# Kernel tuning notes

Hardware: AMD Instinct MI355X
Metric: run time of the kernel (lower is better)

Reference implementation:

```python
import jax, jax.numpy as jnp
import numpy as np
from jax import lax

TOP_K = 8
EPS = 1e-12


def l2_normalize(x, axis):
    sq = jnp.sum(x * x, axis=axis, keepdims=True)
    return x * lax.rsqrt(jnp.maximum(sq, EPS))


def setup_inputs() -> dict:
    key = jax.random.key(0)
    k1, k2, k3, k4 = jax.random.split(key, 4)
    B, N, C = 256, 197, 768
    POOL, LEN = 1024, 8
    x_embed = jax.random.normal(k1, (B, N, C), dtype=jnp.float32)
    prompt = jax.random.uniform(k2, (POOL, LEN, C), dtype=jnp.float32, minval=-1.0, maxval=1.0)
    prompt_key = jax.random.uniform(k3, (POOL, C), dtype=jnp.float32, minval=-1.0, maxval=1.0)
    # kaiming_normal fan_out: std = sqrt(2 / fan_out)
    proj_w = jax.random.normal(k4, (C, C), dtype=jnp.float32) * np.sqrt(2.0 / C).astype(np.float32)
    proj_b = jnp.zeros((C,), dtype=jnp.float32)
    return {"x_embed": x_embed, "prompt": prompt, "prompt_key": prompt_key,
            "proj_w": proj_w, "proj_b": proj_b}


def reference(x_embed, prompt, prompt_key, proj_w, proj_b):
    B = x_embed.shape[0]
    # embedding_key == 'mean'
    x_mean = jnp.mean(x_embed, axis=1)                     # [B, C]
    prompt_norm = l2_normalize(prompt_key, axis=1)         # [P, C]
    x_norm = l2_normalize(x_mean, axis=1)                  # [B, C]
    similarity = x_norm @ prompt_norm.T                    # [B, P]
    _, idx = lax.top_k(similarity, TOP_K)                  # [B, K]
    # gather prompts: [B, K, L, C] -> [B, K*L, C]
    bp = prompt[idx]
    Bk, K, L, C = bp.shape
    batched_prompt = bp.reshape(Bk, K * L, C)
    # projection + residual (dropout in eval mode = identity)
    batched_prompt = batched_prompt @ proj_w.T + proj_b + batched_prompt
    # key loss term
    batched_key_norm = prompt_norm[idx]                    # [B, K, C]
    reduce_sim = jnp.sum(batched_key_norm * x_norm[:, None, :]) / B
    prompted = jnp.concatenate([x_embed[:, :1, :], batched_prompt, x_embed[:, 1:, :]], axis=1)
    return prompted, reduce_sim
```

## Files before the change

kernel.cpp:

```cpp
#include <hip/hip_runtime.h>
#include <float.h>
#include <math.h>

#define B_    256
#define N_    197
#define C_    768
#define POOL_ 1024
#define LEN_  8
#define TOPK_ 8
#define PROWS (POOL_*LEN_)
#define OUTROWS 261

typedef __attribute__((ext_vector_type(8))) short short8_t;
typedef __attribute__((ext_vector_type(4))) float f32x4;

static const size_t OFF_XMEAN = 0;
static const size_t OFF_XNORM = 786432;
static const size_t OFF_PNORM = 1572864;
static const size_t OFF_SIM   = 4718592;
static const size_t OFF_IDX   = 5767168;
static const size_t OFF_ACC   = 5775360;
static const size_t OFF_ABF   = 5775616;
static const size_t OFF_WBF   = 18358528;
static const size_t OFF_PROJ  = 19538176;

__global__ __launch_bounds__(256) void k1_mean_copy(const float* __restrict__ x,
                                                    float* __restrict__ out,
                                                    float* __restrict__ xmean) {
    int b   = blockIdx.x / 3;
    int seg = blockIdx.x % 3;
    int t = threadIdx.x;
    int r = t >> 6;
    int c = t & 63;
    int c4 = seg * 64 + c;
    const float4* xin  = (const float4*)x   + (size_t)b * (N_ * 192) + c4;
    float4*       outb = (float4*)out       + (size_t)b * (OUTROWS * 192) + c4;

    float sx = 0.f, sy = 0.f, sz = 0.f, sw = 0.f;
    #pragma unroll 7
    for (int n = r; n < 196; n += 4) {
        float4 v = xin[(size_t)n * 192];
        sx += v.x; sy += v.y; sz += v.z; sw += v.w;
        int orow = (n == 0) ? 0 : (64 + n);
        outb[(size_t)orow * 192] = v;
    }
    if (r == 0) {
        float4 v = xin[(size_t)196 * 192];
        sx += v.x; sy += v.y; sz += v.z; sw += v.w;
        outb[(size_t)260 * 192] = v;
    }
    __shared__ float4 red[4][64];
    float4 s; s.x = sx; s.y = sy; s.z = sz; s.w = sw;
    red[r][c] = s;
    __syncthreads();
    if (r == 0) {
        float4 a = red[0][c], b2 = red[1][c], c2 = red[2][c], d = red[3][c];
        const float inv = 1.0f / (float)N_;
        float4 m;
        m.x = (a.x + b2.x + c2.x + d.x) * inv;
        m.y = (a.y + b2.y + c2.y + d.y) * inv;
        m.z = (a.z + b2.z + c2.z + d.z) * inv;
        m.w = (a.w + b2.w + c2.w + d.w) * inv;
        ((float4*)xmean)[b * 192 + c4] = m;
    }
}

__global__ __launch_bounds__(256) void k2_normalize(const float* __restrict__ xmean,
                                                    const float* __restrict__ pkey,
                                                    float* __restrict__ xnorm,
                                                    float* __restrict__ pnorm,
                                                    float* __restrict__ sim_accum) {
    __shared__ float red[256];
    int r = blockIdx.x;
    const float* src; float* dst;
    if (r < B_) { src = xmean + (size_t)r * C_; dst = xnorm + (size_t)r * C_; }
    else        { src = pkey  + (size_t)(r - B_) * C_; dst = pnorm + (size_t)(r - B_) * C_; }
    int t = threadIdx.x;
    float v0 = src[t], v1 = src[t + 256], v2 = src[t + 512];
    red[t] = v0*v0 + v1*v1 + v2*v2;
    __syncthreads();
    for (int off = 128; off > 0; off >>= 1) {
        if (t < off) red[t] += red[t + off];
        __syncthreads();
    }
    float inv = 1.0f / sqrtf(fmaxf(red[0], 1e-12f));
    dst[t] = v0 * inv; dst[t + 256] = v1 * inv; dst[t + 512] = v2 * inv;
    if (r == 0 && t == 0) sim_accum[0] = 0.0f;
}

__device__ __forceinline__ unsigned short f2bf(float f) {
    unsigned int u = __float_as_uint(f);
    u += 0x7fffu + ((u >> 16) & 1u);
    return (unsigned short)(u >> 16);
}
__global__ __launch_bounds__(256) void k2b_convert(const float* __restrict__ prompt,
                                                   const float* __restrict__ projw,
                                                   unsigned short* __restrict__ Abf,
                                                   unsigned short* __restrict__ Wbf) {
    int i4 = blockIdx.x * 256 + threadIdx.x;
    float4 v; unsigned short* d;
    if (i4 < (PROWS * C_ / 4)) {
        v = ((const float4*)prompt)[i4];
        d = Abf + (size_t)i4 * 4;
    } else {
        int j4 = i4 - PROWS * C_ / 4;
        v = ((const float4*)projw)[j4];
        d = Wbf + (size_t)j4 * 4;
    }
    ushort4 o; o.x = f2bf(v.x); o.y = f2bf(v.y); o.z = f2bf(v.z); o.w = f2bf(v.w);
    *(ushort4*)d = o;
}

__global__ __launch_bounds__(256) void k3_sim(const float* __restrict__ xnorm,
                                              const float* __restrict__ pnorm,
                                              float* __restrict__ sim) {
    __shared__ float As[32][33];
    __shared__ float Bs[32][33];
    int t = threadIdx.x;
    int m0 = blockIdx.y * 32, n0 = blockIdx.x * 32;
    int lrow = t >> 3, lc = (t & 7) * 4;
    int ty = t >> 4, tx = t & 15;
    float a00 = 0.f, a01 = 0.f, a10 = 0.f, a11 = 0.f;
    for (int k0 = 0; k0 < C_; k0 += 32) {
        float4 va = *(const float4*)&xnorm[(size_t)(m0 + lrow) * C_ + k0 + lc];
        float4 vb = *(const float4*)&pnorm[(size_t)(n0 + lrow) * C_ + k0 + lc];
        __syncthreads();
        As[lrow][lc] = va.x; As[lrow][lc+1] = va.y; As[lrow][lc+2] = va.z; As[lrow][lc+3] = va.w;
        Bs[lrow][lc] = vb.x; Bs[lrow][lc+1] = vb.y; Bs[lrow][lc+2] = vb.z; Bs[lrow][lc+3] = vb.w;
        __syncthreads();
        #pragma unroll
        for (int kk = 0; kk < 32; ++kk) {
            float a0 = As[ty*2][kk],   a1 = As[ty*2+1][kk];
            float b0 = Bs[tx*2][kk],   b1 = Bs[tx*2+1][kk];
            a00 += a0*b0; a01 += a0*b1; a10 += a1*b0; a11 += a1*b1;
        }
    }
    sim[(size_t)(m0 + ty*2    ) * POOL_ + n0 + tx*2    ] = a00;
    sim[(size_t)(m0 + ty*2    ) * POOL_ + n0 + tx*2 + 1] = a01;
    sim[(size_t)(m0 + ty*2 + 1) * POOL_ + n0 + tx*2    ] = a10;
    sim[(size_t)(m0 + ty*2 + 1) * POOL_ + n0 + tx*2 + 1] = a11;
}

__global__ __launch_bounds__(256) void k4_topk(const float* __restrict__ sim,
                                               int* __restrict__ idx,
                                               float* __restrict__ sim_accum) {
    __shared__ float vals[POOL_];
    __shared__ float wv[4];
    __shared__ int   wi[4];
    int b = blockIdx.x, t = threadIdx.x;
    int wave = t >> 6;
    #pragma unroll
    for (int i = 0; i < 4; ++i) vals[t + 256*i] = sim[(size_t)b * POOL_ + t + 256*i];
    __syncthreads();
    float sumv = 0.0f;
    for (int k = 0; k < TOPK_; ++k) {
        float bv = -FLT_MAX; int bi = POOL_;
        #pragma unroll
        for (int i = 0; i < 4; ++i) {
            int n = t + 256*i;
            float v = vals[n];
            if (v > bv) { bv = v; bi = n; }
        }
        #pragma unroll
        for (int off = 32; off > 0; off >>= 1) {
            float v2 = __shfl_down(bv, off);
            int   i2 = __shfl_down(bi, off);
            if (v2 > bv || (v2 == bv && i2 < bi)) { bv = v2; bi = i2; }
        }
        if ((t & 63) == 0) { wv[wave] = bv; wi[wave] = bi; }
        __syncthreads();
        if (t == 0) {
            float fv = wv[0]; int fi = wi[0];
            #pragma unroll
            for (int w = 1; w < 4; ++w) {
                float v2 = wv[w]; int i2 = wi[w];
                if (v2 > fv || (v2 == fv && i2 < fi)) { fv = v2; fi = i2; }
            }
            idx[b*TOPK_ + k] = fi;
            sumv += fv;
            vals[fi] = -FLT_MAX;
        }
        __syncthreads();
    }
    if (t == 0) atomicAdd(sim_accum, sumv);
}

__global__ __launch_bounds__(256) void k5_gemm(const unsigned short* __restrict__ A,
                                               const unsigned short* __restrict__ W,
                                               const float* __restrict__ bias,
                                               const float* __restrict__ resid,
                                               float* __restrict__ out) {
    __shared__ short As[64*32];
    __shared__ short Bs[128*32];
    const int tid = threadIdx.x;
    const int m0 = blockIdx.y * 64, n0 = blockIdx.x * 128;
    const int wave = tid >> 6, lane = tid & 63;
    const int quad = lane >> 4, lr = lane & 15;
    const int srow = tid >> 2;
    const int scol = (tid & 3) * 8;

    f32x4 acc[4][2] = {};

    for (int kt = 0; kt < 24; ++kt) {
        const int k0 = kt * 32;
        __syncthreads();
        __builtin_amdgcn_global_load_lds(
            (const __attribute__((address_space(1))) void*)&A[(size_t)(m0 + srow) * C_ + k0 + scol],
            (__attribute__((address_space(3))) void*)&As[srow*32 + scol], 16, 0, 0);
        __builtin_amdgcn_global_load_lds(
            (const __attribute__((address_space(1))) void*)&W[(size_t)(n0 + srow) * C_ + k0 + scol],
            (__attribute__((address_space(3))) void*)&Bs[srow*32 + scol], 16, 0, 0);
        __builtin_amdgcn_global_load_lds(
            (const __attribute__((address_space(1))) void*)&W[(size_t)(n0 + 64 + srow) * C_ + k0 + scol],
            (__attribute__((address_space(3))) void*)&Bs[(64 + srow)*32 + scol], 16, 0, 0);
        __syncthreads();

        short8_t af[4], bf[2];
        #pragma unroll
        for (int i = 0; i < 4; ++i)
            af[i] = *(const short8_t*)&As[(i*16 + lr)*32 + quad*8];
        #pragma unroll
        for (int j = 0; j < 2; ++j)
            bf[j] = *(const short8_t*)&Bs[(wave*32 + j*16 + lr)*32 + quad*8];
        #pragma unroll
        for (int i = 0; i < 4; ++i)
            #pragma unroll
            for (int j = 0; j < 2; ++j)
                acc[i][j] = __builtin_amdgcn_mfma_f32_16x16x32_bf16(af[i], bf[j], acc[i][j], 0, 0, 0);
    }

    #pragma unroll
    for (int j = 0; j < 2; ++j) {
        const int n = n0 + wave*32 + j*16 + lr;
        const float bn = bias[n];
        #pragma unroll
        for (int i = 0; i < 4; ++i) {
            const int mbase = m0 + i*16 + quad*4;
            #pragma unroll
            for (int r = 0; r < 4; ++r) {
                const int m = mbase + r;
                out[(size_t)m * C_ + n] = acc[i][j][r] + bn + resid[(size_t)m * C_ + n];
            }
        }
    }
}

__global__ __launch_bounds__(64) void k6_gather(const float* __restrict__ projall,
                                                const int* __restrict__ idx,
                                                const float* __restrict__ sim_accum,
                                                float* __restrict__ out) {
    int row = blockIdx.x;
    int b = row >> 6, j = row & 63;
    int k = j >> 3, l = j & 7;
    int p = idx[b * TOPK_ + k];
    const float4* src = (const float4*)projall + (size_t)(p * LEN_ + l) * 192;
    float4* dst = (float4*)out + (size_t)(b * OUTROWS + 1 + j) * 192;
    int t = threadIdx.x;
    dst[t]       = src[t];
    dst[t + 64]  = src[t + 64];
    dst[t + 128] = src[t + 128];
    if (row == 0 && t == 0)
        out[(size_t)B_ * OUTROWS * C_] = sim_accum[0] * (1.0f / (float)B_);
}

extern "C" void kernel_launch(void* const* d_in, const int* in_sizes, int n_in,
                              void* d_out, int out_size, void* d_ws, size_t ws_size,
                              hipStream_t stream) {
    const float* x_embed = (const float*)d_in[0];
    const float* prompt  = (const float*)d_in[1];
    const float* pkey    = (const float*)d_in[2];
    const float* projw   = (const float*)d_in[3];
    const float* projb   = (const float*)d_in[4];
    float* out = (float*)d_out;
    char* ws = (char*)d_ws;

    float*          xmean   = (float*)(ws + OFF_XMEAN);
    float*          xnorm   = (float*)(ws + OFF_XNORM);
    float*          pnorm   = (float*)(ws + OFF_PNORM);
    float*          sim     = (float*)(ws + OFF_SIM);
    int*            idxp    = (int*)(ws + OFF_IDX);
    float*          acc     = (float*)(ws + OFF_ACC);
    unsigned short* Abf     = (unsigned short*)(ws + OFF_ABF);
    unsigned short* Wbf     = (unsigned short*)(ws + OFF_WBF);
    float*          projall = (float*)(ws + OFF_PROJ);

    k1_mean_copy<<<B_ * 3, 256, 0, stream>>>(x_embed, out, xmean);
    k2_normalize<<<B_ + POOL_, 256, 0, stream>>>(xmean, pkey, xnorm, pnorm, acc);
    k2b_convert<<<(PROWS * C_ / 4 + 768 * 768 / 4) / 256, 256, 0, stream>>>(prompt, projw, Abf, Wbf);
    k3_sim<<<dim3(POOL_ / 32, B_ / 32), 256, 0, stream>>>(xnorm, pnorm, sim);
    k4_topk<<<B_, 256, 0, stream>>>(sim, idxp, acc);
    k5_gemm<<<dim3(C_ / 128, PROWS / 64), 256, 0, stream>>>(Abf, Wbf, projb, prompt, projall);
    k6_gather<<<B_ * 64, 64, 0, stream>>>(projall, idxp, acc, out);
}
```

Measured before the change: 424.1 us.

## Double-buffer GEMM, fuse normalize/convert kernels, nontemporal copies, vectorize sim tile

Several independent changes land together. The projection GEMM gets a two-stage LDS double buffer, so the next tile's global-to-LDS loads overlap the MFMA compute and one barrier per iteration is dropped. The normalize and bf16-convert kernels are merged into a single launch, and the x_embed copy and gather stores use nontemporal loads and stores. The similarity GEMM adds a register prefetch and float4 LDS accesses with padding, and the gather kernel packs four rows per 256-thread block.

```diff
diff --git a/kernel.cpp b/kernel.cpp
--- a/kernel.cpp
+++ b/kernel.cpp
@@ -33,59 +33,36 @@
     int r = t >> 6;
     int c = t & 63;
     int c4 = seg * 64 + c;
-    const float4* xin  = (const float4*)x   + (size_t)b * (N_ * 192) + c4;
-    float4*       outb = (float4*)out       + (size_t)b * (OUTROWS * 192) + c4;
+    const f32x4* xin  = (const f32x4*)x   + (size_t)b * (N_ * 192) + c4;
+    f32x4*       outb = (f32x4*)out       + (size_t)b * (OUTROWS * 192) + c4;
 
     float sx = 0.f, sy = 0.f, sz = 0.f, sw = 0.f;
     #pragma unroll 7
     for (int n = r; n < 196; n += 4) {
-        float4 v = xin[(size_t)n * 192];
+        f32x4 v = __builtin_nontemporal_load(&xin[(size_t)n * 192]);
         sx += v.x; sy += v.y; sz += v.z; sw += v.w;
         int orow = (n == 0) ? 0 : (64 + n);
-        outb[(size_t)orow * 192] = v;
+        __builtin_nontemporal_store(v, &outb[(size_t)orow * 192]);
     }
     if (r == 0) {
-        float4 v = xin[(size_t)196 * 192];
+        f32x4 v = __builtin_nontemporal_load(&xin[(size_t)196 * 192]);
         sx += v.x; sy += v.y; sz += v.z; sw += v.w;
-        outb[(size_t)260 * 192] = v;
-    }
-    __shared__ float4 red[4][64];
-    float4 s; s.x = sx; s.y = sy; s.z = sz; s.w = sw;
+        __builtin_nontemporal_store(v, &outb[(size_t)260 * 192]);
+    }
+    __shared__ f32x4 red[4][64];
+    f32x4 s; s.x = sx; s.y = sy; s.z = sz; s.w = sw;
     red[r][c] = s;
     __syncthreads();
     if (r == 0) {
-        float4 a = red[0][c], b2 = red[1][c], c2 = red[2][c], d = red[3][c];
+        f32x4 a = red[0][c], b2 = red[1][c], c2 = red[2][c], d = red[3][c];
         const float inv = 1.0f / (float)N_;
-        float4 m;
+        f32x4 m;
         m.x = (a.x + b2.x + c2.x + d.x) * inv;
         m.y = (a.y + b2.y + c2.y + d.y) * inv;
         m.z = (a.z + b2.z + c2.z + d.z) * inv;
         m.w = (a.w + b2.w + c2.w + d.w) * inv;
-        ((float4*)xmean)[b * 192 + c4] = m;
-    }
-}
-
-__global__ __launch_bounds__(256) void k2_normalize(const float* __restrict__ xmean,
-                                                    const float* __restrict__ pkey,
-                                                    float* __restrict__ xnorm,
-                                                    float* __restrict__ pnorm,
-                                                    float* __restrict__ sim_accum) {
-    __shared__ float red[256];
-    int r = blockIdx.x;
-    const float* src; float* dst;
-    if (r < B_) { src = xmean + (size_t)r * C_; dst = xnorm + (size_t)r * C_; }
-    else        { src = pkey  + (size_t)(r - B_) * C_; dst = pnorm + (size_t)(r - B_) * C_; }
-    int t = threadIdx.x;
-    float v0 = src[t], v1 = src[t + 256], v2 = src[t + 512];
-    red[t] = v0*v0 + v1*v1 + v2*v2;
-    __syncthreads();
-    for (int off = 128; off > 0; off >>= 1) {
-        if (t < off) red[t] += red[t + off];
-        __syncthreads();
-    }
-    float inv = 1.0f / sqrtf(fmaxf(red[0], 1e-12f));
-    dst[t] = v0 * inv; dst[t + 256] = v1 * inv; dst[t + 512] = v2 * inv;
-    if (r == 0 && t == 0) sim_accum[0] = 0.0f;
+        ((f32x4*)xmean)[b * 192 + c4] = m;
+    }
 }
 
 __device__ __forceinline__ unsigned short f2bf(float f) {
@@ -93,46 +70,79 @@
     u += 0x7fffu + ((u >> 16) & 1u);
     return (unsigned short)(u >> 16);
 }
-__global__ __launch_bounds__(256) void k2b_convert(const float* __restrict__ prompt,
-                                                   const float* __restrict__ projw,
-                                                   unsigned short* __restrict__ Abf,
-                                                   unsigned short* __restrict__ Wbf) {
-    int i4 = blockIdx.x * 256 + threadIdx.x;
-    float4 v; unsigned short* d;
-    if (i4 < (PROWS * C_ / 4)) {
-        v = ((const float4*)prompt)[i4];
-        d = Abf + (size_t)i4 * 4;
+__global__ __launch_bounds__(256) void k2_norm_convert(const float* __restrict__ xmean,
+                                                       const float* __restrict__ pkey,
+                                                       float* __restrict__ xnorm,
+                                                       float* __restrict__ pnorm,
+                                                       float* __restrict__ sim_accum,
+                                                       const float* __restrict__ prompt,
+                                                       const float* __restrict__ projw,
+                                                       unsigned short* __restrict__ Abf,
+                                                       unsigned short* __restrict__ Wbf) {
+    int r = blockIdx.x;
+    int t = threadIdx.x;
+    if (r < B_ + POOL_) {
+        __shared__ float red[256];
+        const float* src; float* dst;
+        if (r < B_) { src = xmean + (size_t)r * C_; dst = xnorm + (size_t)r * C_; }
+        else        { src = pkey  + (size_t)(r - B_) * C_; dst = pnorm + (size_t)(r - B_) * C_; }
+        float v0 = src[t], v1 = src[t + 256], v2 = src[t + 512];
+        red[t] = v0*v0 + v1*v1 + v2*v2;
+        __syncthreads();
+        for (int off = 128; off > 0; off >>= 1) {
+            if (t < off) red[t] += red[t + off];
+            __syncthreads();
+        }
+        float inv = 1.0f / sqrtf(fmaxf(red[0], 1e-12f));
+        dst[t] = v0 * inv; dst[t + 256] = v1 * inv; dst[t + 512] = v2 * inv;
+        if (r == 0 && t == 0) sim_accum[0] = 0.0f;
     } else {
-        int j4 = i4 - PROWS * C_ / 4;
-        v = ((const float4*)projw)[j4];
-        d = Wbf + (size_t)j4 * 4;
-    }
-    ushort4 o; o.x = f2bf(v.x); o.y = f2bf(v.y); o.z = f2bf(v.z); o.w = f2bf(v.w);
-    *(ushort4*)d = o;
+        int i4 = (r - (B_ + POOL_)) * 256 + t;
+        float4 v; unsigned short* d;
+        if (i4 < (PROWS * C_ / 4)) {
+            v = ((const float4*)prompt)[i4];
+            d = Abf + (size_t)i4 * 4;
+        } else {
+            int j4 = i4 - PROWS * C_ / 4;
+            v = ((const float4*)projw)[j4];
+            d = Wbf + (size_t)j4 * 4;
+        }
+        ushort4 o; o.x = f2bf(v.x); o.y = f2bf(v.y); o.z = f2bf(v.z); o.w = f2bf(v.w);
+        *(ushort4*)d = o;
+    }
 }
 
 __global__ __launch_bounds__(256) void k3_sim(const float* __restrict__ xnorm,
                                               const float* __restrict__ pnorm,
                                               float* __restrict__ sim) {
-    __shared__ float As[32][33];
-    __shared__ float Bs[32][33];
+    __shared__ float As[32][36];
+    __shared__ float Bs[32][36];
     int t = threadIdx.x;
     int m0 = blockIdx.y * 32, n0 = blockIdx.x * 32;
     int lrow = t >> 3, lc = (t & 7) * 4;
     int ty = t >> 4, tx = t & 15;
     float a00 = 0.f, a01 = 0.f, a10 = 0.f, a11 = 0.f;
+    float4 va = *(const float4*)&xnorm[(size_t)(m0 + lrow) * C_ + lc];
+    float4 vb = *(const float4*)&pnorm[(size_t)(n0 + lrow) * C_ + lc];
     for (int k0 = 0; k0 < C_; k0 += 32) {
-        float4 va = *(const float4*)&xnorm[(size_t)(m0 + lrow) * C_ + k0 + lc];
-        float4 vb = *(const float4*)&pnorm[(size_t)(n0 + lrow) * C_ + k0 + lc];
-        __syncthreads();
-        As[lrow][lc] = va.x; As[lrow][lc+1] = va.y; As[lrow][lc+2] = va.z; As[lrow][lc+3] = va.w;
-        Bs[lrow][lc] = vb.x; Bs[lrow][lc+1] = vb.y; Bs[lrow][lc+2] = vb.z; Bs[lrow][lc+3] = vb.w;
-        __syncthreads();
-        #pragma unroll
-        for (int kk = 0; kk < 32; ++kk) {
-            float a0 = As[ty*2][kk],   a1 = As[ty*2+1][kk];
-            float b0 = Bs[tx*2][kk],   b1 = Bs[tx*2+1][kk];
-            a00 += a0*b0; a01 += a0*b1; a10 += a1*b0; a11 += a1*b1;
+        __syncthreads();
+        *(float4*)&As[lrow][lc] = va;
+        *(float4*)&Bs[lrow][lc] = vb;
+        __syncthreads();
+        if (k0 + 32 < C_) {
+            va = *(const float4*)&xnorm[(size_t)(m0 + lrow) * C_ + k0 + 32 + lc];
+            vb = *(const float4*)&pnorm[(size_t)(n0 + lrow) * C_ + k0 + 32 + lc];
+        }
+        #pragma unroll
+        for (int kk = 0; kk < 32; kk += 4) {
+            float4 A0 = *(const float4*)&As[ty*2][kk];
+            float4 A1 = *(const float4*)&As[ty*2+1][kk];
+            float4 B0 = *(const float4*)&Bs[tx*2][kk];
+            float4 B1 = *(const float4*)&Bs[tx*2+1][kk];
+            a00 += A0.x*B0.x; a00 += A0.y*B0.y; a00 += A0.z*B0.z; a00 += A0.w*B0.w;
+            a01 += A0.x*B1.x; a01 += A0.y*B1.y; a01 += A0.z*B1.z; a01 += A0.w*B1.w;
+            a10 += A1.x*B0.x; a10 += A1.y*B0.y; a10 += A1.z*B0.z; a10 += A1.w*B0.w;
+            a11 += A1.x*B1.x; a11 += A1.y*B1.y; a11 += A1.z*B1.z; a11 += A1.w*B1.w;
         }
     }
     sim[(size_t)(m0 + ty*2    ) * POOL_ + n0 + tx*2    ] = a00;
@@ -190,8 +200,8 @@
                                                const float* __restrict__ bias,
                                                const float* __restrict__ resid,
                                                float* __restrict__ out) {
-    __shared__ short As[64*32];
-    __shared__ short Bs[128*32];
+    __shared__ short As[2][64*32];
+    __shared__ short Bs[2][128*32];
     const int tid = threadIdx.x;
     const int m0 = blockIdx.y * 64, n0 = blockIdx.x * 128;
     const int wave = tid >> 6, lane = tid & 63;
@@ -201,33 +211,43 @@
 
     f32x4 acc[4][2] = {};
 
-    for (int kt = 0; kt < 24; ++kt) {
+    auto stage = [&](int buf, int kt) {
         const int k0 = kt * 32;
-        __syncthreads();
         __builtin_amdgcn_global_load_lds(
             (const __attribute__((address_space(1))) void*)&A[(size_t)(m0 + srow) * C_ + k0 + scol],
-            (__attribute__((address_space(3))) void*)&As[srow*32 + scol], 16, 0, 0);
+            (__attribute__((address_space(3))) void*)&As[buf][srow*32 + scol], 16, 0, 0);
         __builtin_amdgcn_global_load_lds(
             (const __attribute__((address_space(1))) void*)&W[(size_t)(n0 + srow) * C_ + k0 + scol],
-            (__attribute__((address_space(3))) void*)&Bs[srow*32 + scol], 16, 0, 0);
+            (__attribute__((address_space(3))) void*)&Bs[buf][srow*32 + scol], 16, 0, 0);
         __builtin_amdgcn_global_load_lds(
             (const __attribute__((address_space(1))) void*)&W[(size_t)(n0 + 64 + srow) * C_ + k0 + scol],
-            (__attribute__((address_space(3))) void*)&Bs[(64 + srow)*32 + scol], 16, 0, 0);
-        __syncthreads();
-
+            (__attribute__((address_space(3))) void*)&Bs[buf][(64 + srow)*32 + scol], 16, 0, 0);
+    };
+    auto compute = [&](int buf) {
         short8_t af[4], bf[2];
         #pragma unroll
         for (int i = 0; i < 4; ++i)
-            af[i] = *(const short8_t*)&As[(i*16 + lr)*32 + quad*8];
+            af[i] = *(const short8_t*)&As[buf][(i*16 + lr)*32 + quad*8];
         #pragma unroll
         for (int j = 0; j < 2; ++j)
-            bf[j] = *(const short8_t*)&Bs[(wave*32 + j*16 + lr)*32 + quad*8];
+            bf[j] = *(const short8_t*)&Bs[buf][(wave*32 + j*16 + lr)*32 + quad*8];
         #pragma unroll
         for (int i = 0; i < 4; ++i)
             #pragma unroll
             for (int j = 0; j < 2; ++j)
                 acc[i][j] = __builtin_amdgcn_mfma_f32_16x16x32_bf16(af[i], bf[j], acc[i][j], 0, 0, 0);
-    }
+    };
+
+    stage(0, 0);
+    __syncthreads();
+    int cur = 0;
+    for (int kt = 0; kt < 23; ++kt) {
+        stage(cur ^ 1, kt + 1);
+        compute(cur);
+        __syncthreads();
+        cur ^= 1;
+    }
+    compute(cur);
 
     #pragma unroll
     for (int j = 0; j < 2; ++j) {
@@ -245,20 +265,20 @@
     }
 }
 
-__global__ __launch_bounds__(64) void k6_gather(const float* __restrict__ projall,
-                                                const int* __restrict__ idx,
-                                                const float* __restrict__ sim_accum,
-                                                float* __restrict__ out) {
-    int row = blockIdx.x;
+__global__ __launch_bounds__(256) void k6_gather(const float* __restrict__ projall,
+                                                 const int* __restrict__ idx,
+                                                 const float* __restrict__ sim_accum,
+                                                 float* __restrict__ out) {
+    int row = blockIdx.x * 4 + (threadIdx.x >> 6);
+    int t = threadIdx.x & 63;
     int b = row >> 6, j = row & 63;
     int k = j >> 3, l = j & 7;
     int p = idx[b * TOPK_ + k];
-    const float4* src = (const float4*)projall + (size_t)(p * LEN_ + l) * 192;
-    float4* dst = (float4*)out + (size_t)(b * OUTROWS + 1 + j) * 192;
-    int t = threadIdx.x;
-    dst[t]       = src[t];
-    dst[t + 64]  = src[t + 64];
-    dst[t + 128] = src[t + 128];
+    const f32x4* src = (const f32x4*)projall + (size_t)(p * LEN_ + l) * 192;
+    f32x4* dst = (f32x4*)out + (size_t)(b * OUTROWS + 1 + j) * 192;
+    __builtin_nontemporal_store(src[t],       &dst[t]);
+    __builtin_nontemporal_store(src[t + 64],  &dst[t + 64]);
+    __builtin_nontemporal_store(src[t + 128], &dst[t + 128]);
     if (row == 0 && t == 0)
         out[(size_t)B_ * OUTROWS * C_] = sim_accum[0] * (1.0f / (float)B_);
 }
@@ -284,11 +304,12 @@
     unsigned short* Wbf     = (unsigned short*)(ws + OFF_WBF);
     float*          projall = (float*)(ws + OFF_PROJ);
 
+    const int convBlocks = (PROWS * C_ / 4 + 768 * 768 / 4) / 256;
     k1_mean_copy<<<B_ * 3, 256, 0, stream>>>(x_embed, out, xmean);
-    k2_normalize<<<B_ + POOL_, 256, 0, stream>>>(xmean, pkey, xnorm, pnorm, acc);
-    k2b_convert<<<(PROWS * C_ / 4 + 768 * 768 / 4) / 256, 256, 0, stream>>>(prompt, projw, Abf, Wbf);
+    k2_norm_convert<<<B_ + POOL_ + convBlocks, 256, 0, stream>>>(xmean, pkey, xnorm, pnorm, acc,
+                                                                 prompt, projw, Abf, Wbf);
     k3_sim<<<dim3(POOL_ / 32, B_ / 32), 256, 0, stream>>>(xnorm, pnorm, sim);
     k4_topk<<<B_, 256, 0, stream>>>(sim, idxp, acc);
     k5_gemm<<<dim3(C_ / 128, PROWS / 64), 256, 0, stream>>>(Abf, Wbf, projb, prompt, projall);
-    k6_gather<<<B_ * 64, 64, 0, stream>>>(projall, idxp, acc, out);
-}
+    k6_gather<<<B_ * 64 / 4, 256, 0, stream>>>(projall, idxp, acc, out);
+}
```

New measurement: 408.9 us. -3.6%, faster.
